# Optimization experiments

Hardware: AMD Instinct MI355X
Metric: run time of the kernel (lower is better)

## Reference

```python
import jax, jax.numpy as jnp
import numpy as np

B, N, IN_DIM, H, D = 16, 1024, 128, 4, 64
NEG_SLOPE = 0.2


def setup_inputs() -> dict:
    key = jax.random.key(0)
    k1, k2, k3, k4, k5 = jax.random.split(key, 5)
    x = jax.random.normal(k1, (B, N, IN_DIM), dtype=jnp.float32)
    adj = jax.random.randint(k2, (N, N), 0, 2, dtype=jnp.int32)
    adj = adj.at[jnp.arange(N), jnp.arange(N)].set(1)  # self-loops so no empty softmax row
    # xavier-uniform-ish scales
    w_lim = float(np.sqrt(6.0 / (IN_DIM + H * D)))
    a_lim = float(np.sqrt(6.0 / (H + D)))
    W = jax.random.uniform(k3, (IN_DIM, H * D), minval=-w_lim, maxval=w_lim, dtype=jnp.float32)
    a_src = jax.random.uniform(k4, (H, D), minval=-a_lim, maxval=a_lim, dtype=jnp.float32)
    a_dst = jax.random.uniform(k5, (H, D), minval=-a_lim, maxval=a_lim, dtype=jnp.float32)
    return {"x": x, "adj": adj, "W": W, "a_src": a_src, "a_dst": a_dst}


def reference(x, adj, W, a_src, a_dst):
    b, n, _ = x.shape
    h = (x @ W).reshape(b, n, H, D)                       # (B,N,H,D)
    e_src = jnp.einsum('bnhd,hd->bnh', h, a_src)          # (B,N,H)
    e_dst = jnp.einsum('bnhd,hd->bnh', h, a_dst)
    e = e_src[:, :, None, :] + e_dst[:, None, :, :]       # (B,N,N,H)
    e = jnp.where(e >= 0, e, NEG_SLOPE * e)               # leaky relu
    mask = (adj > 0)[None, :, :, None]                    # (1,N,N,1)
    e = jnp.where(mask, e, -jnp.inf)
    alpha = jax.nn.softmax(e, axis=2)                     # softmax over neighbors j
    h_out = jnp.einsum('bijh,bjhd->bihd', alpha, h)       # (B,N,H,D)
    return h_out.reshape(b, n, H * D)                     # concat heads
```

## Files before the change

kernel.cpp:

```cpp
#include <hip/hip_runtime.h>
#include <hip/hip_cooperative_groups.h>

namespace cg = cooperative_groups;


#define B_  16
#define N_  1024
#define IND 128
#define H_  4
#define D_  64
#define NEG 0.2f

typedef __attribute__((ext_vector_type(8))) short short8;
typedef __attribute__((ext_vector_type(4))) float float4v;
typedef __attribute__((ext_vector_type(4))) unsigned int uint4v;
typedef __attribute__((ext_vector_type(2))) unsigned int uint2v;

union S8U4 { uint4v u; short8 s; };

static __device__ __forceinline__ unsigned short f2bf(float f) {
  unsigned int u = __float_as_uint(f);
  u += 0x7fffu + ((u >> 16) & 1u);
  return (unsigned short)(u >> 16);
}
static __device__ __forceinline__ unsigned pk_rne(float a, float b) {
  unsigned ua = __float_as_uint(a), ub = __float_as_uint(b);
  ua += 0x7fffu + ((ua >> 16) & 1u);
  ub += 0x7fffu + ((ub >> 16) & 1u);
  return __builtin_amdgcn_perm(ub, ua, 0x07060302);
}

__global__ __launch_bounds__(256) void k_prep(const int* __restrict__ adj,
                                              const float* __restrict__ W,
                                              unsigned int* __restrict__ adjb,
                                              unsigned short* __restrict__ wT) {
  const int g = blockIdx.x, t = threadIdx.x, l = t & 63;
  if (g < 4096) {
    int f = g * 256 + t;
    unsigned long long m = __ballot(adj[f] > 0);
    if (l == 0) {
      adjb[f >> 5] = (unsigned int)m;
      adjb[(f >> 5) + 1] = (unsigned int)(m >> 32);
    }
  } else {
    int wb = g - 4096;
#pragma unroll
    for (int i = 0; i < 4; ++i) {
      int k = wb * 4 + i;
      wT[t * 128 + k] = f2bf(W[k * 256 + t]);
    }
  }
}

__global__ __launch_bounds__(256) void k_proj(const float* __restrict__ x,
                                              const float* __restrict__ a_src,
                                              const float* __restrict__ a_dst,
                                              const unsigned short* __restrict__ wT,
                                              unsigned short* __restrict__ hT,
                                              float* __restrict__ e_srcT,
                                              float* __restrict__ e_dstT) {
  __shared__ unsigned short wbuf[128 * 136];
  const int g = blockIdx.x, t = threadIdx.x;
  const int mt = g >> 1, nh = g & 1;
  const int w = t >> 6, l = t & 63, quad = l >> 4, ln = l & 15;

#pragma unroll
  for (int i = 0; i < 8; ++i) {
    int c = i * 256 + t;
    int n = c >> 4, k8 = c & 15;
    *reinterpret_cast<short8*>(&wbuf[n * 136 + k8 * 8]) =
        *reinterpret_cast<const short8*>(wT + (size_t)(nh * 128 + n) * 128 + k8 * 8);
  }
  __syncthreads();

  const int m0 = mt * 64 + w * 16;
  short8 afr[4];
#pragma unroll
  for (int ks = 0; ks < 4; ++ks) {
    const float* xp = x + (size_t)(m0 + ln) * IND + ks * 32 + quad * 8;
    float4v x0 = *reinterpret_cast<const float4v*>(xp);
    float4v x1 = *reinterpret_cast<const float4v*>(xp + 4);
    S8U4 cvt;
    cvt.u = (uint4v){pk_rne(x0.x, x0.y), pk_rne(x0.z, x0.w),
                     pk_rne(x1.x, x1.y), pk_rne(x1.z, x1.w)};
    afr[ks] = cvt.s;
  }

  float4v acc[8];
#pragma unroll
  for (int nf = 0; nf < 8; ++nf) acc[nf] = (float4v){0.f, 0.f, 0.f, 0.f};
#pragma unroll
  for (int nf = 0; nf < 8; ++nf) {
#pragma unroll
    for (int ks = 0; ks < 4; ++ks) {
      short8 bv = *reinterpret_cast<const short8*>(
          &wbuf[(nf * 16 + ln) * 136 + ks * 32 + quad * 8]);
      acc[nf] = __builtin_amdgcn_mfma_f32_16x16x32_bf16(afr[ks], bv, acc[nf], 0, 0, 0);
    }
  }

  const int m_base = m0 + quad * 4;
  const int b = m_base >> 10, nl = m_base & 1023;
  const int jb = nl >> 3, jo = nl & 7;
#pragma unroll
  for (int hl = 0; hl < 2; ++hl) {
    const int h = nh * 2 + hl;
    float es[4] = {0.f, 0.f, 0.f, 0.f}, ed[4] = {0.f, 0.f, 0.f, 0.f};
#pragma unroll
    for (int n4 = 0; n4 < 4; ++n4) {
      int nf = hl * 4 + n4;
      int col = nh * 128 + nf * 16 + ln;
      float asv = a_src[col], adv = a_dst[col];
#pragma unroll
      for (int r = 0; r < 4; ++r) { es[r] += acc[nf][r] * asv; ed[r] += acc[nf][r] * adv; }
      uint2v hv;
      hv.x = pk_rne(acc[nf][0], acc[nf][1]);
      hv.y = pk_rne(acc[nf][2], acc[nf][3]);
      int d = n4 * 16 + ln;
      *reinterpret_cast<uint2v*>(hT + ((size_t)(b * H_ + h) * 128 + jb) * 512 + d * 8 + jo) = hv;
    }
#pragma unroll
    for (int r = 0; r < 4; ++r) {
#pragma unroll
      for (int msk = 1; msk < 16; msk <<= 1) {
        es[r] += __shfl_xor(es[r], msk, 64);
        ed[r] += __shfl_xor(ed[r], msk, 64);
      }
    }
    if (ln == 0) {
#pragma unroll
      for (int r = 0; r < 4; ++r) {
        e_srcT[(b * H_ + h) * N_ + nl + r] = es[r];
        e_dstT[(b * H_ + h) * N_ + nl + r] = ed[r];
      }
    }
  }
}

__global__ __launch_bounds__(256) void k_attn(const unsigned short* __restrict__ hT,
                                              const float* __restrict__ e_srcT,
                                              const float* __restrict__ e_dstT,
                                              const unsigned int* __restrict__ adjb,
                                              float* __restrict__ out) {
  __shared__ float F1[H_][N_];
  __shared__ float F2[H_][N_];
  __shared__ float es_lds[H_][16];
  __shared__ unsigned int adj_lds[16 * 33];

  const int t = threadIdx.x;
  const int w = t >> 6;
  const int l = t & 63;
  const int quad = l >> 4;
  const int ln = l & 15;
  const int b = blockIdx.x >> 6;
  const int i0 = (blockIdx.x & 63) * 16;

#pragma unroll
  for (int q = 0; q < 2; ++q) {
    int idx = q * 256 + t;
    adj_lds[(idx >> 5) * 33 + (idx & 31)] = adjb[(i0 + (idx >> 5)) * 32 + (idx & 31)];
  }
#pragma unroll
  for (int q = 0; q < 2; ++q) {
    int idx = q * 256 + t;
    int hidx = idx >> 7, j = (idx & 127) * 8;
    const float* ep = e_dstT + (size_t)(b * H_ + hidx) * N_ + j;
    float4v e0 = *reinterpret_cast<const float4v*>(ep);
    float4v e1 = *reinterpret_cast<const float4v*>(ep + 4);
    *reinterpret_cast<float4v*>(&F1[hidx][j]) =
        (float4v){__expf(e0.x), __expf(e0.y), __expf(e0.z), __expf(e0.w)};
    *reinterpret_cast<float4v*>(&F1[hidx][j + 4]) =
        (float4v){__expf(e1.x), __expf(e1.y), __expf(e1.z), __expf(e1.w)};
    *reinterpret_cast<float4v*>(&F2[hidx][j]) =
        (float4v){__expf(NEG * e0.x), __expf(NEG * e0.y), __expf(NEG * e0.z), __expf(NEG * e0.w)};
    *reinterpret_cast<float4v*>(&F2[hidx][j + 4]) =
        (float4v){__expf(NEG * e1.x), __expf(NEG * e1.y), __expf(NEG * e1.z), __expf(NEG * e1.w)};
  }
  if (l < 16) es_lds[w][l] = e_srcT[(size_t)(b * H_ + w) * N_ + i0 + l];
  __syncthreads();

  const float cc = es_lds[w][ln];
  const float E1 = __expf(cc), E2 = __expf(NEG * cc);

  const unsigned short* slab = hT + (size_t)(b * H_ + w) * 65536;
  const int doff = (quad * 512) + ln * 8;
  float4v acc[4];
#pragma unroll
  for (int dt = 0; dt < 4; ++dt) acc[dt] = (float4v){0.f, 0.f, 0.f, 0.f};
  float ds = 0.f;

  for (int j0 = 0; j0 < N_; j0 += 32) {
    const float* f1p = &F1[w][j0 + quad * 8];
    const float* f2p = &F2[w][j0 + quad * 8];
    float4v f1a = *reinterpret_cast<const float4v*>(f1p);
    float4v f1b = *reinterpret_cast<const float4v*>(f1p + 4);
    float4v f2a = *reinterpret_cast<const float4v*>(f2p);
    float4v f2b = *reinterpret_cast<const float4v*>(f2p + 4);
    float f1[8] = {f1a.x, f1a.y, f1a.z, f1a.w, f1b.x, f1b.y, f1b.z, f1b.w};
    float f2[8] = {f2a.x, f2a.y, f2a.z, f2a.w, f2b.x, f2b.y, f2b.z, f2b.w};
    unsigned int aw = adj_lds[ln * 33 + (j0 >> 5)];
    short8 afr;
#pragma unroll
    for (int jj = 0; jj < 8; ++jj) {
      float p = fmaxf(E1 * f1[jj], E2 * f2[jj]);
      p = ((aw >> (quad * 8 + jj)) & 1u) ? p : 0.f;
      ds += p;
      afr[jj] = (short)f2bf(p);
    }
    const unsigned short* jbase = slab + (size_t)(j0 >> 3) * 512;
#pragma unroll
    for (int dt = 0; dt < 4; ++dt) {
      short8 bv = *reinterpret_cast<const short8*>(jbase + doff + dt * 128);
      acc[dt] = __builtin_amdgcn_mfma_f32_16x16x32_bf16(afr, bv, acc[dt], 0, 0, 0);
    }
  }

  float d2 = ds + __shfl_xor(ds, 16, 64);
  d2 += __shfl_xor(d2, 32, 64);
  float inv[4];
#pragma unroll
  for (int r = 0; r < 4; ++r)
    inv[r] = 1.0f / fmaxf(__shfl(d2, quad * 4 + r, 64), 1e-30f);

#pragma unroll
  for (int dt = 0; dt < 4; ++dt) {
#pragma unroll
    for (int r = 0; r < 4; ++r) {
      int row = i0 + quad * 4 + r;
      int col = w * 64 + dt * 16 + ln;
      out[(size_t)(b * N_ + row) * 256 + col] = acc[dt][r] * inv[r];
    }
  }
}

__global__ __launch_bounds__(256) void k_gat(const float* x, const int* adj,
                                             const float* W, const float* a_src,
                                             const float* a_dst, float* out) {
  __shared__ float xls[IND * 8];
  __shared__ float e_lds[H_][N_];
  __shared__ float es_lds2[H_][64];
  __shared__ unsigned int adj_lds2[64 * 33];

  const int g = blockIdx.x, t = threadIdx.x, l = t & 63, wv = t >> 6;
  unsigned short* hT = reinterpret_cast<unsigned short*>(out);
  float* e_srcT = out + 2097152;
  float* e_dstT = out + 2162688;
  unsigned int* adjb = reinterpret_cast<unsigned int*>(out + 2228224);

#pragma unroll 4
  for (int q = 0; q < 16; ++q) {
    int f = g * 4096 + q * 256 + t;
    unsigned long long m = __ballot(adj[f] > 0);
    if (l == 0) { adjb[f >> 5] = (unsigned int)m; adjb[(f >> 5) + 1] = (unsigned int)(m >> 32); }
  }
  const int hh = wv, d = l;
  const float asv = a_src[t], adv = a_dst[t];
  for (int u = 0; u < 8; ++u) {
    const int vb = g * 8 + u, b = vb >> 7, n0 = (vb & 127) * 8;
    {
      const float4v v = reinterpret_cast<const float4v*>(x + (size_t)(b * N_ + n0) * IND)[t];
      int e0 = t * 4, r = e0 >> 7, k = e0 & 127;
      float* dst = &xls[k * 8 + r];
      dst[0] = v.x; dst[8] = v.y; dst[16] = v.z; dst[24] = v.w;
    }
    __syncthreads();
    float acc[8] = {0.f, 0.f, 0.f, 0.f, 0.f, 0.f, 0.f, 0.f};
#pragma unroll 4
    for (int k = 0; k < IND; ++k) {
      float wval = W[k * 256 + t];
      const float4v x0 = *reinterpret_cast<const float4v*>(&xls[k * 8]);
      const float4v x1 = *reinterpret_cast<const float4v*>(&xls[k * 8 + 4]);
      acc[0] += x0.x * wval; acc[1] += x0.y * wval; acc[2] += x0.z * wval; acc[3] += x0.w * wval;
      acc[4] += x1.x * wval; acc[5] += x1.y * wval; acc[6] += x1.z * wval; acc[7] += x1.w * wval;
    }
    short8 hs;
#pragma unroll
    for (int r = 0; r < 8; ++r) hs[r] = (short)f2bf(acc[r]);
    *reinterpret_cast<short8*>(hT + ((size_t)(b * H_ + hh) * D_ + d) * N_ + n0) = hs;
#pragma unroll
    for (int r = 0; r < 8; ++r) {
      float es = acc[r] * asv, ed = acc[r] * adv;
#pragma unroll
      for (int m = 1; m < 64; m <<= 1) { es += __shfl_xor(es, m, 64); ed += __shfl_xor(ed, m, 64); }
      if (d == 0) {
        e_srcT[(b * H_ + hh) * N_ + n0 + r] = es;
        e_dstT[(b * H_ + hh) * N_ + n0 + r] = ed;
      }
    }
    __syncthreads();
  }
  cg::this_grid().sync();
  const int w = wv, quad = l >> 4, ln = l & 15, b = g >> 4, i0 = (g & 15) * 64;
#pragma unroll
  for (int q = 0; q < 8; ++q) {
    int idx = q * 256 + t, r = idx >> 5, c2 = idx & 31;
    adj_lds2[r * 33 + c2] = adjb[(i0 + r) * 32 + c2];
  }
  {
    const float4v* src = reinterpret_cast<const float4v*>(e_dstT + (size_t)(b * H_ + w) * N_);
    float4v* dst = reinterpret_cast<float4v*>(&e_lds[w][0]);
#pragma unroll
    for (int q = 0; q < 4; ++q) dst[q * 64 + l] = src[q * 64 + l];
    es_lds2[w][l] = e_srcT[(size_t)(b * H_ + w) * N_ + i0 + l];
  }
  __syncthreads();
  float c[4];
#pragma unroll
  for (int it = 0; it < 4; ++it) c[it] = es_lds2[w][it * 16 + ln];
  const unsigned short* slab = hT + (size_t)(b * H_ + w) * D_ * N_;
  const unsigned short* hb = slab + ln * N_;
  float4v acc[4][4];
#pragma unroll
  for (int it = 0; it < 4; ++it)
#pragma unroll
    for (int dt = 0; dt < 4; ++dt) acc[it][dt] = (float4v){0.f, 0.f, 0.f, 0.f};
  float ds[4] = {0.f, 0.f, 0.f, 0.f};
  for (int j0 = 0; j0 < N_; j0 += 32) {
    const float* ep = &e_lds[w][j0 + quad * 8];
    float4v e0 = *reinterpret_cast<const float4v*>(ep);
    float4v e1 = *reinterpret_cast<const float4v*>(ep + 4);
    float ej[8] = {e0.x, e0.y, e0.z, e0.w, e1.x, e1.y, e1.z, e1.w};
    unsigned int aw[4];
#pragma unroll
    for (int it = 0; it < 4; ++it) aw[it] = adj_lds2[(it * 16 + ln) * 33 + (j0 >> 5)];
    short8 afr[4];
#pragma unroll
    for (int it = 0; it < 4; ++it) {
#pragma unroll
      for (int jj = 0; jj < 8; ++jj) {
        float s = c[it] + ej[jj];
        s = fmaxf(s, NEG * s); s = fminf(s, 30.f);
        float p = ((aw[it] >> (quad * 8 + jj)) & 1u) ? __expf(s) : 0.f;
        ds[it] += p; afr[it][jj] = (short)f2bf(p);
      }
    }
#pragma unroll
    for (int dt = 0; dt < 4; ++dt) {
      short8 bv = *reinterpret_cast<const short8*>(hb + dt * 16 * N_ + j0 + quad * 8);
#pragma unroll
      for (int it = 0; it < 4; ++it)
        acc[it][dt] = __builtin_amdgcn_mfma_f32_16x16x32_bf16(afr[it], bv, acc[it][dt], 0, 0, 0);
    }
  }
  float inv[4][4];
#pragma unroll
  for (int it = 0; it < 4; ++it) {
    float d2 = ds[it] + __shfl_xor(ds[it], 16, 64);
    d2 += __shfl_xor(d2, 32, 64);
#pragma unroll
    for (int r = 0; r < 4; ++r) inv[it][r] = 1.0f / fmaxf(__shfl(d2, quad * 4 + r, 64), 1e-30f);
  }
  cg::this_grid().sync();
#pragma unroll
  for (int it = 0; it < 4; ++it)
#pragma unroll
    for (int dt = 0; dt < 4; ++dt)
#pragma unroll
      for (int r = 0; r < 4; ++r) {
        int row = i0 + it * 16 + quad * 4 + r, col = w * 64 + dt * 16 + ln;
        out[(size_t)(b * N_ + row) * 256 + col] = acc[it][dt][r] * inv[it][r];
      }
}

extern "C" void kernel_launch(void* const* d_in, const int* in_sizes, int n_in,
                              void* d_out, int out_size, void* d_ws, size_t ws_size,
                              hipStream_t stream) {
  const float* x = (const float*)d_in[0];
  const int* adj = (const int*)d_in[1];
  const float* W = (const float*)d_in[2];
  const float* a_src = (const float*)d_in[3];
  const float* a_dst = (const float*)d_in[4];
  float* outp = (float*)d_out;

  if (ws_size >= 9109504u) {
    char* ws = (char*)d_ws;
    unsigned short* hT = (unsigned short*)ws;
    float* e_srcT = (float*)(ws + 8388608);
    float* e_dstT = (float*)(ws + 8650752);
    unsigned int* adjb = (unsigned int*)(ws + 8912896);
    unsigned short* wT = (unsigned short*)(ws + 9043968);
    hipLaunchKernelGGL(k_prep, dim3(4128), dim3(256), 0, stream, adj, W, adjb, wT);
    hipLaunchKernelGGL(k_proj, dim3(512), dim3(256), 0, stream,
                       x, a_src, a_dst, wT, hT, e_srcT, e_dstT);
    hipLaunchKernelGGL(k_attn, dim3(1024), dim3(256), 0, stream,
                       hT, e_srcT, e_dstT, adjb, outp);
  } else {
    void* args[] = {(void*)&x, (void*)&adj, (void*)&W, (void*)&a_src, (void*)&a_dst, (void*)&outp};
    hipLaunchCooperativeKernel((void*)k_gat, dim3(256), dim3(256), args, 0u, stream);
  }
}
```

Baseline: 104.1 us.

## Fuse prep and projection kernels, pack exp tables as bf16 pairs, remap attention blocks

Merges the adjacency bitpacking and projection into one launch. Each projection block now converts W to bf16 itself instead of reading a pre-transposed copy, which removes one kernel launch and the wT buffer. In the attention kernel the two fp32 exp tables become a single table of packed bf16 pairs, halving LDS use, and launch bounds request 4 blocks per CU. Blocks are also remapped so neighbouring block IDs handle different batches. The cost is redundant strided W reads in every projection block and lower precision in the exp factors.

```diff
diff --git a/kernel.cpp b/kernel.cpp
--- a/kernel.cpp
+++ b/kernel.cpp
@@ -30,37 +30,27 @@
   return __builtin_amdgcn_perm(ub, ua, 0x07060302);
 }
 
-__global__ __launch_bounds__(256) void k_prep(const int* __restrict__ adj,
-                                              const float* __restrict__ W,
-                                              unsigned int* __restrict__ adjb,
-                                              unsigned short* __restrict__ wT) {
-  const int g = blockIdx.x, t = threadIdx.x, l = t & 63;
-  if (g < 4096) {
-    int f = g * 256 + t;
+__global__ __launch_bounds__(256) void k_projprep(const float* __restrict__ x,
+                                                  const int* __restrict__ adj,
+                                                  const float* __restrict__ W,
+                                                  const float* __restrict__ a_src,
+                                                  const float* __restrict__ a_dst,
+                                                  unsigned short* __restrict__ hT,
+                                                  float* __restrict__ e_srcT,
+                                                  float* __restrict__ e_dstT,
+                                                  unsigned int* __restrict__ adjb) {
+  const int g = blockIdx.x, t = threadIdx.x;
+  if (g >= 512) {
+    int f = (g - 512) * 256 + t;
     unsigned long long m = __ballot(adj[f] > 0);
-    if (l == 0) {
+    if ((t & 63) == 0) {
       adjb[f >> 5] = (unsigned int)m;
       adjb[(f >> 5) + 1] = (unsigned int)(m >> 32);
     }
-  } else {
-    int wb = g - 4096;
-#pragma unroll
-    for (int i = 0; i < 4; ++i) {
-      int k = wb * 4 + i;
-      wT[t * 128 + k] = f2bf(W[k * 256 + t]);
-    }
-  }
-}
-
-__global__ __launch_bounds__(256) void k_proj(const float* __restrict__ x,
-                                              const float* __restrict__ a_src,
-                                              const float* __restrict__ a_dst,
-                                              const unsigned short* __restrict__ wT,
-                                              unsigned short* __restrict__ hT,
-                                              float* __restrict__ e_srcT,
-                                              float* __restrict__ e_dstT) {
+    return;
+  }
+
   __shared__ unsigned short wbuf[128 * 136];
-  const int g = blockIdx.x, t = threadIdx.x;
   const int mt = g >> 1, nh = g & 1;
   const int w = t >> 6, l = t & 63, quad = l >> 4, ln = l & 15;
 
@@ -68,8 +58,11 @@
   for (int i = 0; i < 8; ++i) {
     int c = i * 256 + t;
     int n = c >> 4, k8 = c & 15;
-    *reinterpret_cast<short8*>(&wbuf[n * 136 + k8 * 8]) =
-        *reinterpret_cast<const short8*>(wT + (size_t)(nh * 128 + n) * 128 + k8 * 8);
+    const float* wp = W + (size_t)(k8 * 8) * 256 + nh * 128 + n;
+    short8 wv8;
+#pragma unroll
+    for (int kk = 0; kk < 8; ++kk) wv8[kk] = (short)f2bf(wp[kk * 256]);
+    *reinterpret_cast<short8*>(&wbuf[n * 136 + k8 * 8]) = wv8;
   }
   __syncthreads();
 
@@ -137,13 +130,12 @@
   }
 }
 
-__global__ __launch_bounds__(256) void k_attn(const unsigned short* __restrict__ hT,
-                                              const float* __restrict__ e_srcT,
-                                              const float* __restrict__ e_dstT,
-                                              const unsigned int* __restrict__ adjb,
-                                              float* __restrict__ out) {
-  __shared__ float F1[H_][N_];
-  __shared__ float F2[H_][N_];
+__global__ __launch_bounds__(256, 4) void k_attn(const unsigned short* __restrict__ hT,
+                                                 const float* __restrict__ e_srcT,
+                                                 const float* __restrict__ e_dstT,
+                                                 const unsigned int* __restrict__ adjb,
+                                                 float* __restrict__ out) {
+  __shared__ unsigned int FP[H_][N_];
   __shared__ float es_lds[H_][16];
   __shared__ unsigned int adj_lds[16 * 33];
 
@@ -152,8 +144,9 @@
   const int l = t & 63;
   const int quad = l >> 4;
   const int ln = l & 15;
-  const int b = blockIdx.x >> 6;
-  const int i0 = (blockIdx.x & 63) * 16;
+  const int g = blockIdx.x;
+  const int b = ((g & 7) << 1) | ((g >> 3) & 1);
+  const int i0 = ((g >> 4) & 63) * 16;
 
 #pragma unroll
   for (int q = 0; q < 2; ++q) {
@@ -167,14 +160,17 @@
     const float* ep = e_dstT + (size_t)(b * H_ + hidx) * N_ + j;
     float4v e0 = *reinterpret_cast<const float4v*>(ep);
     float4v e1 = *reinterpret_cast<const float4v*>(ep + 4);
-    *reinterpret_cast<float4v*>(&F1[hidx][j]) =
-        (float4v){__expf(e0.x), __expf(e0.y), __expf(e0.z), __expf(e0.w)};
-    *reinterpret_cast<float4v*>(&F1[hidx][j + 4]) =
-        (float4v){__expf(e1.x), __expf(e1.y), __expf(e1.z), __expf(e1.w)};
-    *reinterpret_cast<float4v*>(&F2[hidx][j]) =
-        (float4v){__expf(NEG * e0.x), __expf(NEG * e0.y), __expf(NEG * e0.z), __expf(NEG * e0.w)};
-    *reinterpret_cast<float4v*>(&F2[hidx][j + 4]) =
-        (float4v){__expf(NEG * e1.x), __expf(NEG * e1.y), __expf(NEG * e1.z), __expf(NEG * e1.w)};
+    uint4v p0, p1;
+    p0.x = pk_rne(__expf(e0.x), __expf(NEG * e0.x));
+    p0.y = pk_rne(__expf(e0.y), __expf(NEG * e0.y));
+    p0.z = pk_rne(__expf(e0.z), __expf(NEG * e0.z));
+    p0.w = pk_rne(__expf(e0.w), __expf(NEG * e0.w));
+    p1.x = pk_rne(__expf(e1.x), __expf(NEG * e1.x));
+    p1.y = pk_rne(__expf(e1.y), __expf(NEG * e1.y));
+    p1.z = pk_rne(__expf(e1.z), __expf(NEG * e1.z));
+    p1.w = pk_rne(__expf(e1.w), __expf(NEG * e1.w));
+    *reinterpret_cast<uint4v*>(&FP[hidx][j]) = p0;
+    *reinterpret_cast<uint4v*>(&FP[hidx][j + 4]) = p1;
   }
   if (l < 16) es_lds[w][l] = e_srcT[(size_t)(b * H_ + w) * N_ + i0 + l];
   __syncthreads();
@@ -190,19 +186,16 @@
   float ds = 0.f;
 
   for (int j0 = 0; j0 < N_; j0 += 32) {
-    const float* f1p = &F1[w][j0 + quad * 8];
-    const float* f2p = &F2[w][j0 + quad * 8];
-    float4v f1a = *reinterpret_cast<const float4v*>(f1p);
-    float4v f1b = *reinterpret_cast<const float4v*>(f1p + 4);
-    float4v f2a = *reinterpret_cast<const float4v*>(f2p);
-    float4v f2b = *reinterpret_cast<const float4v*>(f2p + 4);
-    float f1[8] = {f1a.x, f1a.y, f1a.z, f1a.w, f1b.x, f1b.y, f1b.z, f1b.w};
-    float f2[8] = {f2a.x, f2a.y, f2a.z, f2a.w, f2b.x, f2b.y, f2b.z, f2b.w};
+    uint4v u0 = *reinterpret_cast<const uint4v*>(&FP[w][j0 + quad * 8]);
+    uint4v u1 = *reinterpret_cast<const uint4v*>(&FP[w][j0 + quad * 8 + 4]);
+    unsigned uu[8] = {u0.x, u0.y, u0.z, u0.w, u1.x, u1.y, u1.z, u1.w};
     unsigned int aw = adj_lds[ln * 33 + (j0 >> 5)];
     short8 afr;
 #pragma unroll
     for (int jj = 0; jj < 8; ++jj) {
-      float p = fmaxf(E1 * f1[jj], E2 * f2[jj]);
+      float f1 = __uint_as_float(uu[jj] << 16);
+      float f2 = __uint_as_float(uu[jj] & 0xffff0000u);
+      float p = fmaxf(E1 * f1, E2 * f2);
       p = ((aw >> (quad * 8 + jj)) & 1u) ? p : 0.f;
       ds += p;
       afr[jj] = (short)f2bf(p);
@@ -372,16 +365,14 @@
   const float* a_dst = (const float*)d_in[4];
   float* outp = (float*)d_out;
 
-  if (ws_size >= 9109504u) {
+  if (ws_size >= 9043968u) {
     char* ws = (char*)d_ws;
     unsigned short* hT = (unsigned short*)ws;
     float* e_srcT = (float*)(ws + 8388608);
     float* e_dstT = (float*)(ws + 8650752);
     unsigned int* adjb = (unsigned int*)(ws + 8912896);
-    unsigned short* wT = (unsigned short*)(ws + 9043968);
-    hipLaunchKernelGGL(k_prep, dim3(4128), dim3(256), 0, stream, adj, W, adjb, wT);
-    hipLaunchKernelGGL(k_proj, dim3(512), dim3(256), 0, stream,
-                       x, a_src, a_dst, wT, hT, e_srcT, e_dstT);
+    hipLaunchKernelGGL(k_projprep, dim3(4608), dim3(256), 0, stream,
+                       x, adj, W, a_src, a_dst, hT, e_srcT, e_dstT, adjb);
     hipLaunchKernelGGL(k_attn, dim3(1024), dim3(256), 0, stream,
                        hT, e_srcT, e_dstT, adjb, outp);
   } else {
```

Result: slower. 125.6 us (+20.6%).
